# Performance work log

Hardware: AMD Instinct MI355X
Metric: run time of the kernel (lower is better)

Reference implementation:

```python
import jax, jax.numpy as jnp
import numpy as np

EPS = 1e-12  # torch F.normalize eps

def _l2norm(t):
    # F.normalize(t, p=2, dim=1): divide by clamped L2 norm
    n = jnp.sqrt(jnp.sum(t * t, axis=1, keepdims=True))
    return t / jnp.maximum(n, EPS)


def setup_inputs() -> dict:
    key = jax.random.key(0)
    k1, k2, k3 = jax.random.split(key, 3)
    N, K, D = 262144, 512, 64
    inputs = jax.random.normal(k1, (N, D), dtype=jnp.float32)
    labels = jax.random.randint(k2, (N,), 0, K, dtype=jnp.int64)
    embedding = jax.random.normal(k3, (K, D), dtype=jnp.float32)
    return {"inputs": inputs, "labels": labels, "embedding": embedding}


def reference(inputs, labels, embedding):
    K, D = embedding.shape
    flat = inputs.reshape(-1, D)  # [N, D]
    # cosine similarity: [N, K]
    distances = _l2norm(flat) @ _l2norm(embedding).T
    encoding_indices = jnp.argmax(distances, axis=1)  # [N]
    encodings = jax.nn.one_hot(encoding_indices, K, dtype=flat.dtype)  # [N, K]
    # quantize lookup via one-hot matmul (as in original)
    quantized = (encodings @ embedding).reshape(inputs.shape)
    # labeled branch: closs = mean(1 - distances[i, labels[i]])
    picked = jnp.take_along_axis(distances, labels[:, None], axis=1)[:, 0]
    loss = jnp.mean(1.0 - picked)
    # straight-through estimator
    quantized = inputs + jax.lax.stop_gradient(quantized - inputs)
    perplexity = jnp.array(1, dtype=jnp.int32)
    return (loss, quantized, perplexity, encodings, encoding_indices[:, None])
```

## Files before the change

### kernel.cpp

```cpp
#include <hip/hip_runtime.h>
#include <math.h>

#define N_ROWS 262144
#define KCODES 512
#define DIM 64
#define BLOCK 256
#define ROWS_PER_BLOCK 128
#define KTILE 64
#define NSTAGES (KCODES / KTILE)
#define LDS_ROW 72
#define PLANE_STRIDE (KTILE * LDS_ROW)

typedef __attribute__((ext_vector_type(8))) short short8;
typedef __attribute__((ext_vector_type(4))) float f4;

static const size_t OFF_LOSS = 0;
static const size_t OFF_Q    = 1;
static const size_t OFF_PERP = 1 + (size_t)N_ROWS * DIM;
static const size_t OFF_ENC  = OFF_PERP + 1;
static const size_t OFF_IDX  = OFF_ENC + (size_t)N_ROWS * KCODES;

__device__ __forceinline__ unsigned short bf16rne(float f) {
    unsigned int u = __float_as_uint(f);
    u = (u + 0x7fffu + ((u >> 16) & 1u)) >> 16;
    return (unsigned short)u;
}
__device__ __forceinline__ float bf16tof(unsigned short h) {
    return __uint_as_float(((unsigned int)h) << 16);
}

__global__ __launch_bounds__(64) void vq_prep(const float* __restrict__ emb,
                                              unsigned short* __restrict__ ph,
                                              unsigned short* __restrict__ pm,
                                              unsigned short* __restrict__ pl,
                                              float* __restrict__ out_loss,
                                              float* __restrict__ out_perp) {
    int k = blockIdx.x;
    int d = threadIdx.x;
    float v = emb[k * DIM + d];
    float s = v * v;
    #pragma unroll
    for (int off = 32; off > 0; off >>= 1) s += __shfl_xor(s, off, 64);
    float vn = v / fmaxf(sqrtf(s), 1e-12f);
    unsigned short h = bf16rne(vn);
    float r = vn - bf16tof(h);
    unsigned short m = bf16rne(r);
    r = r - bf16tof(m);
    unsigned short l = bf16rne(r);
    ph[k * DIM + d] = h;
    pm[k * DIM + d] = m;
    pl[k * DIM + d] = l;
    if (k == 0 && d == 0) { *out_loss = 0.0f; *out_perp = 1.0f; }
}

#define MFMA(A, B, C) C = __builtin_amdgcn_mfma_f32_16x16x32_bf16(A, B, C, 0, 0, 0)

__global__ __launch_bounds__(BLOCK, 3) void vq_main(const float* __restrict__ x,
                                                    const int* __restrict__ labels,
                                                    const float* __restrict__ emb,
                                                    const unsigned short* __restrict__ ph,
                                                    const unsigned short* __restrict__ pm,
                                                    const unsigned short* __restrict__ pl,
                                                    float* __restrict__ out_loss,
                                                    float* __restrict__ out_q,
                                                    float* __restrict__ out_enc,
                                                    float* __restrict__ out_idx) {
    const int tid   = threadIdx.x;
    const int wv    = tid >> 6;
    const int lane  = tid & 63;
    const int q     = lane >> 4;
    const int c     = lane & 15;
    const int wbase = blockIdx.x * ROWS_PER_BLOCK + wv * 32;

    __shared__ __align__(16) unsigned short sE[3 * PLANE_STRIDE];

    float inv_nx[2];
    short8 Ah[2][2], Am[2][2], Al[2][2];
    #pragma unroll
    for (int t = 0; t < 2; ++t) {
        float xv[16];
        const float* xp = x + (size_t)(wbase + t * 16 + c) * DIM + q * 8;
        #pragma unroll
        for (int s = 0; s < 2; ++s) {
            float4 lo = *(const float4*)(xp + s * 32);
            float4 hi = *(const float4*)(xp + s * 32 + 4);
            xv[s * 8 + 0] = lo.x; xv[s * 8 + 1] = lo.y;
            xv[s * 8 + 2] = lo.z; xv[s * 8 + 3] = lo.w;
            xv[s * 8 + 4] = hi.x; xv[s * 8 + 5] = hi.y;
            xv[s * 8 + 6] = hi.z; xv[s * 8 + 7] = hi.w;
        }
        float s2 = 0.f;
        #pragma unroll
        for (int j = 0; j < 16; ++j) s2 = fmaf(xv[j], xv[j], s2);
        s2 += __shfl_xor(s2, 16, 64);
        s2 += __shfl_xor(s2, 32, 64);
        inv_nx[t] = 1.0f / fmaxf(sqrtf(s2), 1e-12f);
        #pragma unroll
        for (int s = 0; s < 2; ++s)
            #pragma unroll
            for (int j = 0; j < 8; ++j) {
                float v = xv[s * 8 + j];
                unsigned short h = bf16rne(v);
                float r = v - bf16tof(h);
                unsigned short m = bf16rne(r);
                r = r - bf16tof(m);
                unsigned short l = bf16rne(r);
                Ah[t][s][j] = (short)h;
                Am[t][s][j] = (short)m;
                Al[t][s][j] = (short)l;
            }
    }

    int   lbl[2][4];
    float best[2][4], pick[2][4];
    int   bidx[2][4];
    #pragma unroll
    for (int t = 0; t < 2; ++t)
        #pragma unroll
        for (int r = 0; r < 4; ++r) {
            lbl[t][r]  = labels[wbase + t * 16 + q * 4 + r];
            best[t][r] = -3.4e38f;
            bidx[t][r] = 0;
            pick[t][r] = 0.f;
        }

    for (int st = 0; st < NSTAGES; ++st) {
        __syncthreads();
        #pragma unroll
        for (int i = 0; i < 2; ++i) {
            int ch = tid + i * BLOCK;
            int code = ch >> 3, part = ch & 7;
            int dst = code * LDS_ROW + part * 8;
            int src = st * (KTILE * DIM) + ch * 8;
            *(float4*)&sE[dst]                    = *(const float4*)(ph + src);
            *(float4*)&sE[PLANE_STRIDE + dst]     = *(const float4*)(pm + src);
            *(float4*)&sE[2 * PLANE_STRIDE + dst] = *(const float4*)(pl + src);
        }
        __syncthreads();

        #pragma unroll 2
        for (int sub = 0; sub < KTILE / 16; ++sub) {
            const unsigned short* bp = &sE[(sub * 16 + c) * LDS_ROW + q * 8];
            short8 Bh0 = *(const short8*)(bp);
            short8 Bh1 = *(const short8*)(bp + 32);
            short8 Bm0 = *(const short8*)(bp + PLANE_STRIDE);
            short8 Bm1 = *(const short8*)(bp + PLANE_STRIDE + 32);
            short8 Bl0 = *(const short8*)(bp + 2 * PLANE_STRIDE);
            short8 Bl1 = *(const short8*)(bp + 2 * PLANE_STRIDE + 32);

            {
                int g = st * (KTILE / 16) + sub;
                float* zb = out_enc + (size_t)(wbase + g) * KCODES;
                f4 z = {0.f, 0.f, 0.f, 0.f};
                __builtin_nontemporal_store(z, (f4*)(zb + lane * 4));
                __builtin_nontemporal_store(z, (f4*)(zb + 256 + lane * 4));
            }

            f4 acc0 = {0.f, 0.f, 0.f, 0.f};
            f4 acc1 = {0.f, 0.f, 0.f, 0.f};
            MFMA(Ah[0][0], Bh0, acc0);  MFMA(Ah[1][0], Bh0, acc1);
            MFMA(Ah[0][1], Bh1, acc0);  MFMA(Ah[1][1], Bh1, acc1);
            MFMA(Ah[0][0], Bm0, acc0);  MFMA(Ah[1][0], Bm0, acc1);
            MFMA(Ah[0][1], Bm1, acc0);  MFMA(Ah[1][1], Bm1, acc1);
            MFMA(Am[0][0], Bh0, acc0);  MFMA(Am[1][0], Bh0, acc1);
            MFMA(Am[0][1], Bh1, acc0);  MFMA(Am[1][1], Bh1, acc1);
            MFMA(Ah[0][0], Bl0, acc0);  MFMA(Ah[1][0], Bl0, acc1);
            MFMA(Ah[0][1], Bl1, acc0);  MFMA(Ah[1][1], Bl1, acc1);
            MFMA(Al[0][0], Bh0, acc0);  MFMA(Al[1][0], Bh0, acc1);
            MFMA(Al[0][1], Bh1, acc0);  MFMA(Al[1][1], Bh1, acc1);
            MFMA(Am[0][0], Bm0, acc0);  MFMA(Am[1][0], Bm0, acc1);
            MFMA(Am[0][1], Bm1, acc0);  MFMA(Am[1][1], Bm1, acc1);

            const int code = st * KTILE + sub * 16 + c;
            #pragma unroll
            for (int r = 0; r < 4; ++r) {
                float d0 = acc0[r];
                if (d0 > best[0][r]) { best[0][r] = d0; bidx[0][r] = code; }
                if (code == lbl[0][r]) pick[0][r] = d0;
                float d1 = acc1[r];
                if (d1 > best[1][r]) { best[1][r] = d1; bidx[1][r] = code; }
                if (code == lbl[1][r]) pick[1][r] = d1;
            }
        }
    }

    asm volatile("s_waitcnt vmcnt(0)" ::: "memory");

    #pragma unroll
    for (int t = 0; t < 2; ++t)
        #pragma unroll
        for (int r = 0; r < 4; ++r) {
            float b = best[t][r]; int i = bidx[t][r]; float p = pick[t][r];
            #pragma unroll
            for (int m = 1; m < 16; m <<= 1) {
                float ob = __shfl_xor(b, m, 64);
                int   oi = __shfl_xor(i, m, 64);
                p += __shfl_xor(p, m, 64);
                if (ob > b || (ob == b && oi < i)) { b = ob; i = oi; }
            }
            bidx[t][r] = i; pick[t][r] = p;
        }

    if (c == 0) {
        #pragma unroll
        for (int t = 0; t < 2; ++t)
            #pragma unroll
            for (int r = 0; r < 4; ++r) {
                int row = wbase + t * 16 + q * 4 + r;
                out_enc[(size_t)row * KCODES + bidx[t][r]] = 1.0f;
                out_idx[row] = (float)bidx[t][r];
            }
    }

    #pragma unroll
    for (int t = 0; t < 2; ++t)
        #pragma unroll
        for (int r = 0; r < 4; ++r) {
            int row = wbase + t * 16 + q * 4 + r;
            f4 v = ((const f4*)(emb + (size_t)bidx[t][r] * DIM))[c];
            __builtin_nontemporal_store(v, ((f4*)(out_q + (size_t)row * DIM)) + c);
        }

    float lv = 0.f;
    #pragma unroll
    for (int t = 0; t < 2; ++t)
        #pragma unroll
        for (int r = 0; r < 4; ++r) {
            float invv = __shfl(inv_nx[t], q * 4 + r, 64);
            lv += (1.0f - pick[t][r] * invv);
        }
    lv *= 1.0f / ((float)N_ROWS * 16.0f);
    #pragma unroll
    for (int m = 1; m < 64; m <<= 1) lv += __shfl_xor(lv, m, 64);
    if (lane == 0) atomicAdd(out_loss, lv);
}

extern "C" void kernel_launch(void* const* d_in, const int* in_sizes, int n_in,
                              void* d_out, int out_size, void* d_ws, size_t ws_size,
                              hipStream_t stream) {
    const float* x      = (const float*)d_in[0];
    const int*   labels = (const int*)d_in[1];
    const float* emb    = (const float*)d_in[2];
    float* out = (float*)d_out;
    unsigned short* ph = (unsigned short*)d_ws;
    unsigned short* pm = ph + (size_t)KCODES * DIM;
    unsigned short* pl = pm + (size_t)KCODES * DIM;

    hipLaunchKernelGGL(vq_prep, dim3(KCODES), dim3(64), 0, stream,
                       emb, ph, pm, pl, out + OFF_LOSS, out + OFF_PERP);
    hipLaunchKernelGGL(vq_main, dim3(N_ROWS / ROWS_PER_BLOCK), dim3(BLOCK), 0, stream,
                       x, labels, emb, ph, pm, pl,
                       out + OFF_LOSS, out + OFF_Q, out + OFF_ENC, out + OFF_IDX);
}
```

Before: 737.4 us.

## Write one-hot rows directly after argmax and split MFMA accumulator chains

The zero-fill of the encoding matrix, previously interleaved with the MFMA loop, is removed. Full one-hot rows are now written once after the argmax reduction, via shuffle-broadcast indices, which drops the separate scattered 1.0 store and the vmcnt wait. Each MFMA dependency chain is split into two independent accumulators that are summed afterwards, to shorten dependent MFMA latency. Launch bounds are raised to 4 blocks per CU, which may force register spills, and the encoding writes no longer overlap with compute.

```diff
diff --git a/kernel.cpp b/kernel.cpp
--- a/kernel.cpp
+++ b/kernel.cpp
@@ -55,7 +55,7 @@
 
 #define MFMA(A, B, C) C = __builtin_amdgcn_mfma_f32_16x16x32_bf16(A, B, C, 0, 0, 0)
 
-__global__ __launch_bounds__(BLOCK, 3) void vq_main(const float* __restrict__ x,
+__global__ __launch_bounds__(BLOCK, 4) void vq_main(const float* __restrict__ x,
                                                     const int* __restrict__ labels,
                                                     const float* __restrict__ emb,
                                                     const unsigned short* __restrict__ ph,
@@ -66,11 +66,10 @@
                                                     float* __restrict__ out_enc,
                                                     float* __restrict__ out_idx) {
     const int tid   = threadIdx.x;
-    const int wv    = tid >> 6;
     const int lane  = tid & 63;
     const int q     = lane >> 4;
     const int c     = lane & 15;
-    const int wbase = blockIdx.x * ROWS_PER_BLOCK + wv * 32;
+    const int wbase = blockIdx.x * ROWS_PER_BLOCK + (tid >> 6) * 32;
 
     __shared__ __align__(16) unsigned short sE[3 * PLANE_STRIDE];
 
@@ -148,43 +147,35 @@
             short8 Bl0 = *(const short8*)(bp + 2 * PLANE_STRIDE);
             short8 Bl1 = *(const short8*)(bp + 2 * PLANE_STRIDE + 32);
 
-            {
-                int g = st * (KTILE / 16) + sub;
-                float* zb = out_enc + (size_t)(wbase + g) * KCODES;
-                f4 z = {0.f, 0.f, 0.f, 0.f};
-                __builtin_nontemporal_store(z, (f4*)(zb + lane * 4));
-                __builtin_nontemporal_store(z, (f4*)(zb + 256 + lane * 4));
-            }
-
-            f4 acc0 = {0.f, 0.f, 0.f, 0.f};
-            f4 acc1 = {0.f, 0.f, 0.f, 0.f};
-            MFMA(Ah[0][0], Bh0, acc0);  MFMA(Ah[1][0], Bh0, acc1);
-            MFMA(Ah[0][1], Bh1, acc0);  MFMA(Ah[1][1], Bh1, acc1);
-            MFMA(Ah[0][0], Bm0, acc0);  MFMA(Ah[1][0], Bm0, acc1);
-            MFMA(Ah[0][1], Bm1, acc0);  MFMA(Ah[1][1], Bm1, acc1);
-            MFMA(Am[0][0], Bh0, acc0);  MFMA(Am[1][0], Bh0, acc1);
-            MFMA(Am[0][1], Bh1, acc0);  MFMA(Am[1][1], Bh1, acc1);
-            MFMA(Ah[0][0], Bl0, acc0);  MFMA(Ah[1][0], Bl0, acc1);
-            MFMA(Ah[0][1], Bl1, acc0);  MFMA(Ah[1][1], Bl1, acc1);
-            MFMA(Al[0][0], Bh0, acc0);  MFMA(Al[1][0], Bh0, acc1);
-            MFMA(Al[0][1], Bh1, acc0);  MFMA(Al[1][1], Bh1, acc1);
-            MFMA(Am[0][0], Bm0, acc0);  MFMA(Am[1][0], Bm0, acc1);
-            MFMA(Am[0][1], Bm1, acc0);  MFMA(Am[1][1], Bm1, acc1);
+            f4 a0a = {0.f, 0.f, 0.f, 0.f};
+            f4 a0b = {0.f, 0.f, 0.f, 0.f};
+            f4 a1a = {0.f, 0.f, 0.f, 0.f};
+            f4 a1b = {0.f, 0.f, 0.f, 0.f};
+            MFMA(Ah[0][0], Bh0, a0a);  MFMA(Ah[0][1], Bh1, a0b);
+            MFMA(Ah[1][0], Bh0, a1a);  MFMA(Ah[1][1], Bh1, a1b);
+            MFMA(Ah[0][0], Bm0, a0a);  MFMA(Ah[0][1], Bm1, a0b);
+            MFMA(Ah[1][0], Bm0, a1a);  MFMA(Ah[1][1], Bm1, a1b);
+            MFMA(Am[0][0], Bh0, a0a);  MFMA(Am[0][1], Bh1, a0b);
+            MFMA(Am[1][0], Bh0, a1a);  MFMA(Am[1][1], Bh1, a1b);
+            MFMA(Ah[0][0], Bl0, a0a);  MFMA(Ah[0][1], Bl1, a0b);
+            MFMA(Ah[1][0], Bl0, a1a);  MFMA(Ah[1][1], Bl1, a1b);
+            MFMA(Al[0][0], Bh0, a0a);  MFMA(Al[0][1], Bh1, a0b);
+            MFMA(Al[1][0], Bh0, a1a);  MFMA(Al[1][1], Bh1, a1b);
+            MFMA(Am[0][0], Bm0, a0a);  MFMA(Am[0][1], Bm1, a0b);
+            MFMA(Am[1][0], Bm0, a1a);  MFMA(Am[1][1], Bm1, a1b);
 
             const int code = st * KTILE + sub * 16 + c;
             #pragma unroll
             for (int r = 0; r < 4; ++r) {
-                float d0 = acc0[r];
+                float d0 = a0a[r] + a0b[r];
                 if (d0 > best[0][r]) { best[0][r] = d0; bidx[0][r] = code; }
                 if (code == lbl[0][r]) pick[0][r] = d0;
-                float d1 = acc1[r];
+                float d1 = a1a[r] + a1b[r];
                 if (d1 > best[1][r]) { best[1][r] = d1; bidx[1][r] = code; }
                 if (code == lbl[1][r]) pick[1][r] = d1;
             }
         }
     }
-
-    asm volatile("s_waitcnt vmcnt(0)" ::: "memory");
 
     #pragma unroll
     for (int t = 0; t < 2; ++t)
@@ -201,13 +192,31 @@
             bidx[t][r] = i; pick[t][r] = p;
         }
 
+    {
+        const int col0 = lane * 4, col1 = 256 + lane * 4;
+        #pragma unroll
+        for (int r32 = 0; r32 < 32; ++r32) {
+            int bi = __shfl(bidx[r32 >> 4][r32 & 3], ((r32 >> 2) & 3) * 16, 64);
+            float* base = out_enc + (size_t)(wbase + r32) * KCODES;
+            f4 v0 = { bi == col0     ? 1.f : 0.f,
+                      bi == col0 + 1 ? 1.f : 0.f,
+                      bi == col0 + 2 ? 1.f : 0.f,
+                      bi == col0 + 3 ? 1.f : 0.f };
+            __builtin_nontemporal_store(v0, (f4*)(base + col0));
+            f4 v1 = { bi == col1     ? 1.f : 0.f,
+                      bi == col1 + 1 ? 1.f : 0.f,
+                      bi == col1 + 2 ? 1.f : 0.f,
+                      bi == col1 + 3 ? 1.f : 0.f };
+            __builtin_nontemporal_store(v1, (f4*)(base + col1));
+        }
+    }
+
     if (c == 0) {
         #pragma unroll
         for (int t = 0; t < 2; ++t)
             #pragma unroll
             for (int r = 0; r < 4; ++r) {
                 int row = wbase + t * 16 + q * 4 + r;
-                out_enc[(size_t)row * KCODES + bidx[t][r]] = 1.0f;
                 out_idx[row] = (float)bidx[t][r];
             }
     }
```

Measured after the change: 711.3 us. 3.5% less time.
